# Kernel optimization log

Hardware: AMD Instinct MI355X
Metric: run time of the kernel (lower is better)

## Reference

```python
import jax, jax.numpy as jnp
import numpy as np

N = 8192
H = 512

def setup_inputs() -> dict:
    key = jax.random.key(0)
    ks = jax.random.split(key, 11)
    s = 1.0 / np.sqrt(H)
    return {
        "q": jax.random.normal(ks[0], (N, H), dtype=jnp.float32),
        "k": jax.random.normal(ks[1], (N, H), dtype=jnp.float32),
        "v": jax.random.normal(ks[2], (N, H), dtype=jnp.float32),
        "Wq": jax.random.uniform(ks[3], (H, H), jnp.float32, -s, s),
        "bq": jax.random.uniform(ks[4], (H,), jnp.float32, -s, s),
        "Wk": jax.random.uniform(ks[5], (H, H), jnp.float32, -s, s),
        "bk": jax.random.uniform(ks[6], (H,), jnp.float32, -s, s),
        "Wv": jax.random.uniform(ks[7], (H, H), jnp.float32, -s, s),
        "bv": jax.random.uniform(ks[8], (H,), jnp.float32, -s, s),
        "Wo": jax.random.uniform(ks[9], (H, H), jnp.float32, -s, s),
        "bo": jax.random.uniform(ks[10], (H,), jnp.float32, -s, s),
    }

def reference(q, k, v, Wq, bq, Wk, bk, Wv, bv, Wo, bo):
    # torch Linear: x @ W.T + b
    qp = q @ Wq.T + bq            # [N, H]
    kp = k @ Wk.T + bk            # [N, H]
    vp = v @ Wv.T + bv            # [N, H]
    weights = qp @ kp.T           # [N, N]  (no 1/sqrt(d) scaling in original)
    normalized = jax.nn.softmax(weights, axis=-1)  # [N, N]
    out = normalized @ vp         # [N, H]
    out = out @ Wo.T + bo         # [N, H]
    return (out, normalized)
```

## Files before the change

kernel.cpp:

```cpp
#include <hip/hip_runtime.h>

typedef unsigned short u16;
typedef _Float16 f16x8 __attribute__((ext_vector_type(8)));
typedef u16 u16x8 __attribute__((ext_vector_type(8)));
typedef float floatx4 __attribute__((ext_vector_type(4)));

#define DEV __device__ __forceinline__

DEV u16 f2h(float f) {
  _Float16 h = (_Float16)f;
  return __builtin_bit_cast(u16, h);
}

typedef __attribute__((address_space(3))) void lds_void_t;
typedef const __attribute__((address_space(1))) void gbl_void_t;

DEV void async16(const void* g, void* l) {
  __builtin_amdgcn_global_load_lds((gbl_void_t*)g, (lds_void_t*)l, 16, 0, 0);
}

template <int N>
DEV void wait_vm() {
  static_assert(N == 0 || N == 3 || N == 4 || N == 6 || N == 8 || N == 9 ||
                    N == 12,
                "add vmcnt literal");
  if constexpr (N == 0) asm volatile("s_waitcnt vmcnt(0)" ::: "memory");
  else if constexpr (N == 3) asm volatile("s_waitcnt vmcnt(3)" ::: "memory");
  else if constexpr (N == 4) asm volatile("s_waitcnt vmcnt(4)" ::: "memory");
  else if constexpr (N == 6) asm volatile("s_waitcnt vmcnt(6)" ::: "memory");
  else if constexpr (N == 8) asm volatile("s_waitcnt vmcnt(8)" ::: "memory");
  else if constexpr (N == 9) asm volatile("s_waitcnt vmcnt(9)" ::: "memory");
  else if constexpr (N == 12) asm volatile("s_waitcnt vmcnt(12)" ::: "memory");
}


__global__ __launch_bounds__(256) void k_cvt16(const float* __restrict__ x,
                                               u16* __restrict__ o, int n4) {
  int i = blockIdx.x * 256 + threadIdx.x;
  if (i >= n4) return;
  float4 v = ((const float4*)x)[i];
  *(ushort4*)&o[4 * (size_t)i] =
      make_ushort4(f2h(v.x), f2h(v.y), f2h(v.z), f2h(v.w));
}


__global__ __launch_bounds__(256) void k_red4(const float* __restrict__ p,
                                              size_t pstride,
                                              u16* __restrict__ o, int n4) {
  int i = blockIdx.x * 256 + threadIdx.x;
  if (i >= n4) return;
  float4 a = ((const float4*)p)[i];
  float4 b = ((const float4*)(p + pstride))[i];
  float4 c = ((const float4*)(p + 2 * pstride))[i];
  float4 d = ((const float4*)(p + 3 * pstride))[i];
  *(ushort4*)&o[4 * (size_t)i] =
      make_ushort4(f2h((a.x + b.x) + (c.x + d.x)),
                   f2h((a.y + b.y) + (c.y + d.y)),
                   f2h((a.z + b.z) + (c.z + d.z)),
                   f2h((a.w + b.w) + (c.w + d.w)));
}


__global__ __launch_bounds__(256) void k_transpose(const u16* __restrict__ in,
                                                   u16* __restrict__ out,
                                                   int R, int C) {
  __shared__ u16 T[64][72];
  int m0 = blockIdx.x * 64;
  int n0 = blockIdx.y * 64;
  int t = threadIdx.x;
#pragma unroll
  for (int i = 0; i < 2; ++i) {
    int lin = i * 2048 + t * 8;
    int r = lin >> 6, c = lin & 63;
    u16x8 d = *(const u16x8*)&in[(size_t)(m0 + r) * C + n0 + c];
#pragma unroll
    for (int j = 0; j < 8; ++j) T[r][c + j] = d[j];
  }
  __syncthreads();
#pragma unroll
  for (int i = 0; i < 2; ++i) {
    int lin = i * 2048 + t * 8;
    int r = lin >> 6, c = lin & 63;
    u16x8 d;
#pragma unroll
    for (int j = 0; j < 8; ++j) d[j] = T[c + j][r];
    *(u16x8*)&out[(size_t)(n0 + r) * R + m0 + c] = d;
  }
}


template <bool WRITEP>
__global__ __launch_bounds__(256) void k_softmax(float* __restrict__ W,
                                                 u16* __restrict__ P) {
  const size_t row = blockIdx.x;
  float4* pv = (float4*)(W + row * 8192);
  const int t = threadIdx.x;
  const int w = t >> 6, l = t & 63;
  float4 v[8];
#pragma unroll
  for (int i = 0; i < 8; ++i) v[i] = pv[i * 256 + t];
  float m = -1e30f;
#pragma unroll
  for (int i = 0; i < 8; ++i)
    m = fmaxf(m, fmaxf(fmaxf(v[i].x, v[i].y), fmaxf(v[i].z, v[i].w)));
#pragma unroll
  for (int o = 32; o >= 1; o >>= 1) m = fmaxf(m, __shfl_xor(m, o, 64));
  __shared__ float redm[4];
  __shared__ float reds[4];
  if (l == 0) redm[w] = m;
  __syncthreads();
  m = fmaxf(fmaxf(redm[0], redm[1]), fmaxf(redm[2], redm[3]));
  float s = 0.f;
#pragma unroll
  for (int i = 0; i < 8; ++i) {
    v[i].x = __expf(v[i].x - m); s += v[i].x;
    v[i].y = __expf(v[i].y - m); s += v[i].y;
    v[i].z = __expf(v[i].z - m); s += v[i].z;
    v[i].w = __expf(v[i].w - m); s += v[i].w;
  }
#pragma unroll
  for (int o = 32; o >= 1; o >>= 1) s += __shfl_xor(s, o, 64);
  if (l == 0) reds[w] = s;
  __syncthreads();
  s = (reds[0] + reds[1]) + (reds[2] + reds[3]);
  float inv = 1.0f / s;
#pragma unroll
  for (int i = 0; i < 8; ++i) {
    v[i].x *= inv; v[i].y *= inv; v[i].z *= inv; v[i].w *= inv;
    pv[i * 256 + t] = v[i];
    if constexpr (WRITEP) {
      *(ushort4*)&P[row * 8192 + (size_t)(i * 256 + t) * 4] =
          make_ushort4(f2h(v[i].x), f2h(v[i].y), f2h(v[i].z), f2h(v[i].w));
    }
  }
}


template <int BN, bool AF32, int OMODE, bool BIAS, int MINW>
__global__ __launch_bounds__(256, MINW)
void k_gemm(const void* A_, const u16* __restrict__ Bh,
            const float* __restrict__ bias, void* C_, int K, int lda, int ldb,
            int ldc, size_t zstride) {
  constexpr int NT = BN / 32;
  constexpr int BCHW = BN / 64;
  constexpr int D = 2;
  constexpr int BC = AF32 ? 1 : (D + 1);
  constexpr int LPI = 2 + BCHW;
  __shared__ alignas(16) u16 Ash[BC][128 * 32];
  __shared__ alignas(16) u16 Bsh[BC][BN * 32];

  const int m0 = blockIdx.x * 128;
  const int n0 = blockIdx.y * BN;
  const int kz = blockIdx.z * K;
  const int tid = threadIdx.x;
  const int w = tid >> 6;
  const int l = tid & 63;
  const int lr = l & 15;
  const int lq = l >> 4;
  const int wr = (w >> 1) * 64;
  const int wc = (w & 1) * (BN / 2);
  const int srow = l >> 2;
  const int scolsw = ((l & 3) ^ ((l >> 3) & 3)) * 8;
  const int sw8 = (lq ^ ((lr >> 1) & 3)) * 8;

  const u16* Ah = (const u16*)A_;
  const float* Af = (const float*)A_;

  floatx4 acc[4][NT] = {};

  if constexpr (!AF32) {
    const int nIter = K / 32;
    auto STAGE = [&](int t, int b) {
      const int k0 = kz + (t < nIter ? t : nIter - 1) * 32;
#pragma unroll
      for (int i = 0; i < 2; ++i) {
        int c = w * 2 + i;
        int row = c * 16 + srow;
        async16(Ah + (size_t)(m0 + row) * lda + k0 + scolsw, &Ash[b][c * 512]);
      }
#pragma unroll
      for (int i = 0; i < BCHW; ++i) {
        int c = w * BCHW + i;
        int row = c * 16 + srow;
        async16(Bh + (size_t)(n0 + row) * ldb + k0 + scolsw, &Bsh[b][c * 512]);
      }
    };

#pragma unroll
    for (int t = 0; t < D; ++t) STAGE(t, t);

    int bcon = 0;
    int bpro = D % BC;
    for (int t = 0; t < nIter; ++t) {
      wait_vm<LPI * (D - 1)>();
      __builtin_amdgcn_s_barrier();
      STAGE(t + D, bpro);

      f16x8 fa[4], fb[NT];
#pragma unroll
      for (int x = 0; x < 4; ++x)
        fa[x] = *(const f16x8*)&Ash[bcon][(wr + x * 16 + lr) * 32 + sw8];
#pragma unroll
      for (int x = 0; x < NT; ++x)
        fb[x] = *(const f16x8*)&Bsh[bcon][(wc + x * 16 + lr) * 32 + sw8];
#pragma unroll
      for (int mt = 0; mt < 4; ++mt)
#pragma unroll
        for (int nt = 0; nt < NT; ++nt)
          acc[mt][nt] = __builtin_amdgcn_mfma_f32_16x16x32_f16(
              fa[mt], fb[nt], acc[mt][nt], 0, 0, 0);

      if (++bcon == BC) bcon = 0;
      if (++bpro == BC) bpro = 0;
    }
  } else {
    for (int k0 = 0; k0 < K; k0 += 32) {
      __syncthreads();
#pragma unroll
      for (int i = 0; i < 2; ++i) {
        int lin = i * 2048 + tid * 8;
        int row = lin >> 5, col = lin & 31;
        const float* g = Af + (size_t)(m0 + row) * lda + k0 + col;
        float4 u0 = *(const float4*)g;
        float4 u1 = *(const float4*)(g + 4);
        u16x8 tv;
        tv[0] = f2h(u0.x); tv[1] = f2h(u0.y); tv[2] = f2h(u0.z); tv[3] = f2h(u0.w);
        tv[4] = f2h(u1.x); tv[5] = f2h(u1.y); tv[6] = f2h(u1.z); tv[7] = f2h(u1.w);
        int slot = (col >> 3) ^ ((row >> 1) & 3);
        *(u16x8*)&Ash[0][row * 32 + slot * 8] = tv;
      }
#pragma unroll
      for (int i = 0; i < BCHW; ++i) {
        int c = w * BCHW + i;
        int row = c * 16 + srow;
        async16(Bh + (size_t)(n0 + row) * ldb + k0 + scolsw, &Bsh[0][c * 512]);
      }
      __syncthreads();

      f16x8 fa[4], fb[NT];
#pragma unroll
      for (int x = 0; x < 4; ++x)
        fa[x] = *(const f16x8*)&Ash[0][(wr + x * 16 + lr) * 32 + sw8];
#pragma unroll
      for (int x = 0; x < NT; ++x)
        fb[x] = *(const f16x8*)&Bsh[0][(wc + x * 16 + lr) * 32 + sw8];
#pragma unroll
      for (int mt = 0; mt < 4; ++mt)
#pragma unroll
        for (int nt = 0; nt < NT; ++nt)
          acc[mt][nt] = __builtin_amdgcn_mfma_f32_16x16x32_f16(
              fa[mt], fb[nt], acc[mt][nt], 0, 0, 0);
    }
  }

  float bv[NT];
#pragma unroll
  for (int nt = 0; nt < NT; ++nt)
    bv[nt] = BIAS ? bias[n0 + wc + nt * 16 + lr] : 0.f;
#pragma unroll
  for (int mt = 0; mt < 4; ++mt)
#pragma unroll
    for (int nt = 0; nt < NT; ++nt)
#pragma unroll
      for (int r = 0; r < 4; ++r) {
        float x = acc[mt][nt][r] + bv[nt];
        int row = m0 + wr + mt * 16 + lq * 4 + r;
        int col = n0 + wc + nt * 16 + lr;
        size_t idx = (size_t)row * ldc + col + blockIdx.z * zstride;
        if constexpr (OMODE == 0) {
          ((float*)C_)[idx] = x;
        } else {
          ((u16*)C_)[idx] = f2h(x);
        }
      }
}


__global__ __launch_bounds__(512, 4)
void k_gemm_av(const u16* __restrict__ Ah, const u16* __restrict__ Bh,
               float* __restrict__ C_, int K, int lda, int ldb, int ldc,
               size_t zstride) {
  constexpr int D = 2;
  constexpr int BC = D + 1;
  constexpr int LPI = 3;
  __shared__ alignas(16) u16 Ash[BC][128 * 32];
  __shared__ alignas(16) u16 Bsh[BC][256 * 32];

  const int m0 = blockIdx.x * 128;
  const int n0 = blockIdx.y * 256;
  const int kz = blockIdx.z * K;
  const int tid = threadIdx.x;
  const int w = tid >> 6;
  const int l = tid & 63;
  const int lr = l & 15;
  const int lq = l >> 4;
  const int wr = (w & 1) * 64;
  const int wc = (w >> 1) * 64;
  const int srow = l >> 2;
  const int scolsw = ((l & 3) ^ ((l >> 3) & 3)) * 8;
  const int sw8 = (lq ^ ((lr >> 1) & 3)) * 8;

  floatx4 acc[4][4] = {};

  const int nIter = K / 32;
  auto STAGE = [&](int t, int b) {
    const int k0 = kz + (t < nIter ? t : nIter - 1) * 32;
    {
      int row = w * 16 + srow;
      async16(Ah + (size_t)(m0 + row) * lda + k0 + scolsw, &Ash[b][w * 512]);
    }
#pragma unroll
    for (int i = 0; i < 2; ++i) {
      int c = w * 2 + i;
      int row = c * 16 + srow;
      async16(Bh + (size_t)(n0 + row) * ldb + k0 + scolsw, &Bsh[b][c * 512]);
    }
  };

#pragma unroll
  for (int t = 0; t < D; ++t) STAGE(t, t);

  int bcon = 0;
  int bpro = D % BC;
  for (int t = 0; t < nIter; ++t) {
    wait_vm<LPI * (D - 1)>();
    __builtin_amdgcn_s_barrier();
    STAGE(t + D, bpro);

    f16x8 fa[4], fb[4];
#pragma unroll
    for (int x = 0; x < 4; ++x)
      fa[x] = *(const f16x8*)&Ash[bcon][(wr + x * 16 + lr) * 32 + sw8];
#pragma unroll
    for (int x = 0; x < 4; ++x)
      fb[x] = *(const f16x8*)&Bsh[bcon][(wc + x * 16 + lr) * 32 + sw8];
#pragma unroll
    for (int mt = 0; mt < 4; ++mt)
#pragma unroll
      for (int nt = 0; nt < 4; ++nt)
        acc[mt][nt] = __builtin_amdgcn_mfma_f32_16x16x32_f16(
            fa[mt], fb[nt], acc[mt][nt], 0, 0, 0);

    if (++bcon == BC) bcon = 0;
    if (++bpro == BC) bpro = 0;
  }

#pragma unroll
  for (int mt = 0; mt < 4; ++mt)
#pragma unroll
    for (int nt = 0; nt < 4; ++nt)
#pragma unroll
      for (int r = 0; r < 4; ++r) {
        int row = m0 + wr + mt * 16 + lq * 4 + r;
        int col = n0 + wc + nt * 16 + lr;
        C_[(size_t)row * ldc + col + blockIdx.z * zstride] = acc[mt][nt][r];
      }
}


extern "C" void kernel_launch(void* const* d_in, const int* in_sizes, int n_in,
                              void* d_out, int out_size, void* d_ws,
                              size_t ws_size, hipStream_t stream) {
  constexpr int N = 8192, H = 512;
  const float* q   = (const float*)d_in[0];
  const float* kin = (const float*)d_in[1];
  const float* v   = (const float*)d_in[2];
  const float* Wq  = (const float*)d_in[3];
  const float* bq  = (const float*)d_in[4];
  const float* Wk  = (const float*)d_in[5];
  const float* bk  = (const float*)d_in[6];
  const float* Wv  = (const float*)d_in[7];
  const float* bv  = (const float*)d_in[8];
  const float* Wo  = (const float*)d_in[9];
  const float* bo  = (const float*)d_in[10];
  float* out  = (float*)d_out;
  float* norm = out + (size_t)N * H;

  char* ws = (char*)d_ws;
  const size_t MB = 1024 * 1024;
  u16* xh   = (u16*)(ws + 0 * MB);
  u16* wb   = (u16*)(ws + 8 * MB);
  u16* qp   = (u16*)(ws + 9 * MB);
  u16* kp   = (u16*)(ws + 17 * MB);
  u16* vp   = (u16*)(ws + 25 * MB);
  u16* vpT  = (u16*)(ws + 33 * MB);
  u16* Pf   = (u16*)(ws + 41 * MB);
  float* pS = (float*)(ws + 169 * MB);
  u16* out0 = vp;

  const bool usePf    = ws_size >= 169 * MB;
  const bool useSplit = ws_size >= 233 * MB;

  dim3 blk(256);

  k_cvt16<<<4096, blk, 0, stream>>>(q, xh, (N * H) / 4);
  k_cvt16<<<256, blk, 0, stream>>>(Wq, wb, (H * H) / 4);
  k_gemm<64, false, 1, true, 2><<<dim3(64, 8), blk, 0, stream>>>(
      xh, wb, bq, qp, H, H, H, H, 0);

  k_cvt16<<<4096, blk, 0, stream>>>(kin, xh, (N * H) / 4);
  k_cvt16<<<256, blk, 0, stream>>>(Wk, wb, (H * H) / 4);
  k_gemm<64, false, 1, true, 2><<<dim3(64, 8), blk, 0, stream>>>(
      xh, wb, bk, kp, H, H, H, H, 0);

  k_cvt16<<<4096, blk, 0, stream>>>(v, xh, (N * H) / 4);
  k_cvt16<<<256, blk, 0, stream>>>(Wv, wb, (H * H) / 4);
  k_gemm<64, false, 1, true, 2><<<dim3(64, 8), blk, 0, stream>>>(
      xh, wb, bv, vp, H, H, H, H, 0);
  k_transpose<<<dim3(128, 8), blk, 0, stream>>>(vp, vpT, N, H);

  k_gemm<128, false, 0, false, 3><<<dim3(64, 64), blk, 0, stream>>>(
      qp, kp, nullptr, norm, H, H, H, N, 0);

  if (usePf)
    k_softmax<true><<<N, blk, 0, stream>>>(norm, Pf);
  else
    k_softmax<false><<<N, blk, 0, stream>>>(norm, nullptr);

  if (usePf && useSplit) {
    k_gemm_av<<<dim3(64, 2, 4), dim3(512), 0, stream>>>(
        Pf, vpT, pS, N / 4, N, N, H, (size_t)N * H);
    k_red4<<<4096, blk, 0, stream>>>(pS, (size_t)N * H, out0, (N * H) / 4);
  } else if (usePf) {
    k_gemm<64, false, 1, false, 4><<<dim3(64, 8), blk, 0, stream>>>(
        Pf, vpT, nullptr, out0, N, N, N, H, 0);
  } else {
    k_gemm<64, true, 1, false, 2><<<dim3(64, 8), blk, 0, stream>>>(
        norm, vpT, nullptr, out0, N, N, N, H, 0);
  }

  k_cvt16<<<256, blk, 0, stream>>>(Wo, wb, (H * H) / 4);
  k_gemm<64, false, 0, true, 2><<<dim3(64, 8), blk, 0, stream>>>(
      out0, wb, bo, out, H, H, H, H, 0);
}
```

Before: 682.9 us.

## Use 256x256 tile, 1024-thread GEMM for QK^T and split-K AV

Replaces the 128x256 AV GEMM kernel with a 256x256-tile, 16-wave kernel and reuses it for both the QK^T score GEMM (previously a 128-tile k_gemm) and the split-K P·V GEMM. Larger tiles raise arithmetic intensity and reduce global/L2 traffic per FLOP, and each thread now issues one A and one B async load per stage (vmcnt 2). In exchange, LDS use grows to about 96 KB per block and there are fewer blocks (1024 for QK, 256 for AV), which can lower occupancy and weaken latency hiding.

```diff
diff --git a/kernel.cpp b/kernel.cpp
--- a/kernel.cpp
+++ b/kernel.cpp
@@ -21,10 +21,11 @@
 
 template <int N>
 DEV void wait_vm() {
-  static_assert(N == 0 || N == 3 || N == 4 || N == 6 || N == 8 || N == 9 ||
-                    N == 12,
+  static_assert(N == 0 || N == 2 || N == 3 || N == 4 || N == 6 || N == 8 ||
+                    N == 9 || N == 12,
                 "add vmcnt literal");
   if constexpr (N == 0) asm volatile("s_waitcnt vmcnt(0)" ::: "memory");
+  else if constexpr (N == 2) asm volatile("s_waitcnt vmcnt(2)" ::: "memory");
   else if constexpr (N == 3) asm volatile("s_waitcnt vmcnt(3)" ::: "memory");
   else if constexpr (N == 4) asm volatile("s_waitcnt vmcnt(4)" ::: "memory");
   else if constexpr (N == 6) asm volatile("s_waitcnt vmcnt(6)" ::: "memory");
@@ -276,17 +277,17 @@
 }
 
 
-__global__ __launch_bounds__(512, 4)
-void k_gemm_av(const u16* __restrict__ Ah, const u16* __restrict__ Bh,
-               float* __restrict__ C_, int K, int lda, int ldb, int ldc,
-               size_t zstride) {
+__global__ __launch_bounds__(1024, 4)
+void k_gemm_big(const u16* __restrict__ Ah, const u16* __restrict__ Bh,
+                float* __restrict__ C_, int K, int lda, int ldb, int ldc,
+                size_t zstride) {
   constexpr int D = 2;
   constexpr int BC = D + 1;
-  constexpr int LPI = 3;
-  __shared__ alignas(16) u16 Ash[BC][128 * 32];
+  constexpr int LPI = 2;
+  __shared__ alignas(16) u16 Ash[BC][256 * 32];
   __shared__ alignas(16) u16 Bsh[BC][256 * 32];
 
-  const int m0 = blockIdx.x * 128;
+  const int m0 = blockIdx.x * 256;
   const int n0 = blockIdx.y * 256;
   const int kz = blockIdx.z * K;
   const int tid = threadIdx.x;
@@ -294,8 +295,8 @@
   const int l = tid & 63;
   const int lr = l & 15;
   const int lq = l >> 4;
-  const int wr = (w & 1) * 64;
-  const int wc = (w >> 1) * 64;
+  const int wrow = (w >> 2) * 64;
+  const int wcol = (w & 3) * 64;
   const int srow = l >> 2;
   const int scolsw = ((l & 3) ^ ((l >> 3) & 3)) * 8;
   const int sw8 = (lq ^ ((lr >> 1) & 3)) * 8;
@@ -305,16 +306,10 @@
   const int nIter = K / 32;
   auto STAGE = [&](int t, int b) {
     const int k0 = kz + (t < nIter ? t : nIter - 1) * 32;
-    {
-      int row = w * 16 + srow;
-      async16(Ah + (size_t)(m0 + row) * lda + k0 + scolsw, &Ash[b][w * 512]);
-    }
-#pragma unroll
-    for (int i = 0; i < 2; ++i) {
-      int c = w * 2 + i;
-      int row = c * 16 + srow;
-      async16(Bh + (size_t)(n0 + row) * ldb + k0 + scolsw, &Bsh[b][c * 512]);
-    }
+    async16(Ah + (size_t)(m0 + w * 16 + srow) * lda + k0 + scolsw,
+            &Ash[b][w * 512]);
+    async16(Bh + (size_t)(n0 + w * 16 + srow) * ldb + k0 + scolsw,
+            &Bsh[b][w * 512]);
   };
 
 #pragma unroll
@@ -330,10 +325,10 @@
     f16x8 fa[4], fb[4];
 #pragma unroll
     for (int x = 0; x < 4; ++x)
-      fa[x] = *(const f16x8*)&Ash[bcon][(wr + x * 16 + lr) * 32 + sw8];
+      fa[x] = *(const f16x8*)&Ash[bcon][(wrow + x * 16 + lr) * 32 + sw8];
 #pragma unroll
     for (int x = 0; x < 4; ++x)
-      fb[x] = *(const f16x8*)&Bsh[bcon][(wc + x * 16 + lr) * 32 + sw8];
+      fb[x] = *(const f16x8*)&Bsh[bcon][(wcol + x * 16 + lr) * 32 + sw8];
 #pragma unroll
     for (int mt = 0; mt < 4; ++mt)
 #pragma unroll
@@ -351,8 +346,8 @@
     for (int nt = 0; nt < 4; ++nt)
 #pragma unroll
       for (int r = 0; r < 4; ++r) {
-        int row = m0 + wr + mt * 16 + lq * 4 + r;
-        int col = n0 + wc + nt * 16 + lr;
+        int row = m0 + wrow + mt * 16 + lq * 4 + r;
+        int col = n0 + wcol + nt * 16 + lr;
         C_[(size_t)row * ldc + col + blockIdx.z * zstride] = acc[mt][nt][r];
       }
 }
@@ -409,8 +404,8 @@
       xh, wb, bv, vp, H, H, H, H, 0);
   k_transpose<<<dim3(128, 8), blk, 0, stream>>>(vp, vpT, N, H);
 
-  k_gemm<128, false, 0, false, 3><<<dim3(64, 64), blk, 0, stream>>>(
-      qp, kp, nullptr, norm, H, H, H, N, 0);
+  k_gemm_big<<<dim3(32, 32), dim3(1024), 0, stream>>>(
+      qp, kp, norm, H, H, H, N, 0);
 
   if (usePf)
     k_softmax<true><<<N, blk, 0, stream>>>(norm, Pf);
@@ -418,7 +413,7 @@
     k_softmax<false><<<N, blk, 0, stream>>>(norm, nullptr);
 
   if (usePf && useSplit) {
-    k_gemm_av<<<dim3(64, 2, 4), dim3(512), 0, stream>>>(
+    k_gemm_big<<<dim3(32, 2, 4), dim3(1024), 0, stream>>>(
         Pf, vpT, pS, N / 4, N, N, H, (size_t)N * H);
     k_red4<<<4096, blk, 0, stream>>>(pS, (size_t)N * H, out0, (N * H) / 4);
   } else if (usePf) {
```

Measured after the change: 690.6 us. No clear change (+1.1%).

## Batch QKV conversions and projections into single launches, reshuffle workspace

Applied to the files above, without the earlier changes.

The input conversions for q/k/v are merged into one three-slice kernel, and all four weight conversions into another. The three projection GEMMs become one batched launch (grid z=3) with a new dedicated 128x64-tile kernel. The workspace is repacked so the split-K attention path needs a smaller buffer, and the intermediate non-split Pf path is dropped. This cuts launch count and lets the projections fill the GPU concurrently; the cost is reusing workspace regions across stages, which depends on their lifetimes not overlapping.

```diff
diff --git a/kernel.cpp b/kernel.cpp
--- a/kernel.cpp
+++ b/kernel.cpp
@@ -21,10 +21,11 @@
 
 template <int N>
 DEV void wait_vm() {
-  static_assert(N == 0 || N == 3 || N == 4 || N == 6 || N == 8 || N == 9 ||
-                    N == 12,
+  static_assert(N == 0 || N == 2 || N == 3 || N == 4 || N == 6 || N == 8 ||
+                    N == 9 || N == 12,
                 "add vmcnt literal");
   if constexpr (N == 0) asm volatile("s_waitcnt vmcnt(0)" ::: "memory");
+  else if constexpr (N == 2) asm volatile("s_waitcnt vmcnt(2)" ::: "memory");
   else if constexpr (N == 3) asm volatile("s_waitcnt vmcnt(3)" ::: "memory");
   else if constexpr (N == 4) asm volatile("s_waitcnt vmcnt(4)" ::: "memory");
   else if constexpr (N == 6) asm volatile("s_waitcnt vmcnt(6)" ::: "memory");
@@ -34,12 +35,33 @@
 }
 
 
-__global__ __launch_bounds__(256) void k_cvt16(const float* __restrict__ x,
-                                               u16* __restrict__ o, int n4) {
+__global__ __launch_bounds__(256) void k_cvt3(const float* __restrict__ a,
+                                              const float* __restrict__ b,
+                                              const float* __restrict__ c,
+                                              u16* __restrict__ o, int n4per) {
+  int z = blockIdx.y;
+  const float* src = (z == 0) ? a : ((z == 1) ? b : c);
+  u16* dst = o + (size_t)z * n4per * 4;
   int i = blockIdx.x * 256 + threadIdx.x;
-  if (i >= n4) return;
-  float4 v = ((const float4*)x)[i];
-  *(ushort4*)&o[4 * (size_t)i] =
+  if (i >= n4per) return;
+  float4 v = ((const float4*)src)[i];
+  *(ushort4*)&dst[4 * (size_t)i] =
+      make_ushort4(f2h(v.x), f2h(v.y), f2h(v.z), f2h(v.w));
+}
+
+__global__ __launch_bounds__(256) void k_cvtw(const float* __restrict__ wq,
+                                              const float* __restrict__ wk,
+                                              const float* __restrict__ wv,
+                                              const float* __restrict__ wo_,
+                                              u16* __restrict__ w3,
+                                              u16* __restrict__ wo, int n4per) {
+  int z = blockIdx.y;
+  const float* src = (z == 0) ? wq : ((z == 1) ? wk : ((z == 2) ? wv : wo_));
+  u16* dst = (z < 3) ? (w3 + (size_t)z * n4per * 4) : wo;
+  int i = blockIdx.x * 256 + threadIdx.x;
+  if (i >= n4per) return;
+  float4 v = ((const float4*)src)[i];
+  *(ushort4*)&dst[4 * (size_t)i] =
       make_ushort4(f2h(v.x), f2h(v.y), f2h(v.z), f2h(v.w));
 }
 
@@ -272,6 +294,96 @@
         } else {
           ((u16*)C_)[idx] = f2h(x);
         }
+      }
+}
+
+
+struct Bias3 { const float* p[3]; };
+
+__global__ __launch_bounds__(256, 2)
+void k_gemm_proj(const u16* __restrict__ A3, const u16* __restrict__ W3,
+                 Bias3 b3, u16* __restrict__ C3) {
+  constexpr int H = 512;
+  constexpr int D = 2, BC = 3, LPI = 3;
+  __shared__ alignas(16) u16 Ash[BC][128 * 32];
+  __shared__ alignas(16) u16 Bsh[BC][64 * 32];
+
+  const int z = blockIdx.z;
+  const u16* Ah = A3 + (size_t)z * 8192 * H;
+  const u16* Bh = W3 + (size_t)z * H * H;
+  const float* bias = b3.p[z];
+  u16* C = C3 + (size_t)z * 8192 * H;
+
+  const int m0 = blockIdx.x * 128;
+  const int n0 = blockIdx.y * 64;
+  const int tid = threadIdx.x;
+  const int w = tid >> 6;
+  const int l = tid & 63;
+  const int lr = l & 15;
+  const int lq = l >> 4;
+  const int wr = (w >> 1) * 64;
+  const int wc = (w & 1) * 32;
+  const int srow = l >> 2;
+  const int scolsw = ((l & 3) ^ ((l >> 3) & 3)) * 8;
+  const int sw8 = (lq ^ ((lr >> 1) & 3)) * 8;
+
+  floatx4 acc[4][2] = {};
+
+  const int nIter = H / 32;
+  auto STAGE = [&](int t, int b) {
+    const int k0 = (t < nIter ? t : nIter - 1) * 32;
+#pragma unroll
+    for (int i = 0; i < 2; ++i) {
+      int c = w * 2 + i;
+      int row = c * 16 + srow;
+      async16(Ah + (size_t)(m0 + row) * H + k0 + scolsw, &Ash[b][c * 512]);
+    }
+    {
+      int row = w * 16 + srow;
+      async16(Bh + (size_t)(n0 + row) * H + k0 + scolsw, &Bsh[b][w * 512]);
+    }
+  };
+
+#pragma unroll
+  for (int t = 0; t < D; ++t) STAGE(t, t);
+
+  int bcon = 0;
+  int bpro = D % BC;
+  for (int t = 0; t < nIter; ++t) {
+    wait_vm<LPI * (D - 1)>();
+    __builtin_amdgcn_s_barrier();
+    STAGE(t + D, bpro);
+
+    f16x8 fa[4], fb[2];
+#pragma unroll
+    for (int x = 0; x < 4; ++x)
+      fa[x] = *(const f16x8*)&Ash[bcon][(wr + x * 16 + lr) * 32 + sw8];
+#pragma unroll
+    for (int x = 0; x < 2; ++x)
+      fb[x] = *(const f16x8*)&Bsh[bcon][(wc + x * 16 + lr) * 32 + sw8];
+#pragma unroll
+    for (int mt = 0; mt < 4; ++mt)
+#pragma unroll
+      for (int nt = 0; nt < 2; ++nt)
+        acc[mt][nt] = __builtin_amdgcn_mfma_f32_16x16x32_f16(
+            fa[mt], fb[nt], acc[mt][nt], 0, 0, 0);
+
+    if (++bcon == BC) bcon = 0;
+    if (++bpro == BC) bpro = 0;
+  }
+
+  float bv[2];
+#pragma unroll
+  for (int nt = 0; nt < 2; ++nt) bv[nt] = bias[n0 + wc + nt * 16 + lr];
+#pragma unroll
+  for (int mt = 0; mt < 4; ++mt)
+#pragma unroll
+    for (int nt = 0; nt < 2; ++nt)
+#pragma unroll
+      for (int r = 0; r < 4; ++r) {
+        int row = m0 + wr + mt * 16 + lq * 4 + r;
+        int col = n0 + wc + nt * 16 + lr;
+        C[(size_t)row * H + col] = f2h(acc[mt][nt][r] + bv[nt]);
       }
 }
 
@@ -378,35 +490,30 @@
 
   char* ws = (char*)d_ws;
   const size_t MB = 1024 * 1024;
-  u16* xh   = (u16*)(ws + 0 * MB);
-  u16* wb   = (u16*)(ws + 8 * MB);
-  u16* qp   = (u16*)(ws + 9 * MB);
-  u16* kp   = (u16*)(ws + 17 * MB);
-  u16* vp   = (u16*)(ws + 25 * MB);
-  u16* vpT  = (u16*)(ws + 33 * MB);
-  u16* Pf   = (u16*)(ws + 41 * MB);
-  float* pS = (float*)(ws + 169 * MB);
-  u16* out0 = vp;
-
-  const bool usePf    = ws_size >= 169 * MB;
-  const bool useSplit = ws_size >= 233 * MB;
+  u16* xh3   = (u16*)(ws + 0 * MB);
+  u16* qkv   = (u16*)(ws + 24 * MB);
+  float* pS  = (float*)(ws + 0 * MB);
+  u16* vpT   = (u16*)(ws + 64 * MB);
+  u16* wb3   = (u16*)(ws + 72 * MB);
+  u16* wbo   = (u16*)(ws + 72 * MB + 3 * (size_t)H * H * 2);
+  u16* out0  = (u16*)(ws + 74 * MB);
+  u16* Pf    = (u16*)(ws + 82 * MB);
+
+  u16* qp = qkv;
+  u16* kp = qkv + (size_t)N * H;
+  u16* vp = qkv + 2 * (size_t)N * H;
+
+  const bool usePf = ws_size >= 210 * MB;
 
   dim3 blk(256);
 
-  k_cvt16<<<4096, blk, 0, stream>>>(q, xh, (N * H) / 4);
-  k_cvt16<<<256, blk, 0, stream>>>(Wq, wb, (H * H) / 4);
-  k_gemm<64, false, 1, true, 2><<<dim3(64, 8), blk, 0, stream>>>(
-      xh, wb, bq, qp, H, H, H, H, 0);
-
-  k_cvt16<<<4096, blk, 0, stream>>>(kin, xh, (N * H) / 4);
-  k_cvt16<<<256, blk, 0, stream>>>(Wk, wb, (H * H) / 4);
-  k_gemm<64, false, 1, true, 2><<<dim3(64, 8), blk, 0, stream>>>(
-      xh, wb, bk, kp, H, H, H, H, 0);
-
-  k_cvt16<<<4096, blk, 0, stream>>>(v, xh, (N * H) / 4);
-  k_cvt16<<<256, blk, 0, stream>>>(Wv, wb, (H * H) / 4);
-  k_gemm<64, false, 1, true, 2><<<dim3(64, 8), blk, 0, stream>>>(
-      xh, wb, bv, vp, H, H, H, H, 0);
+  k_cvt3<<<dim3(4096, 3), blk, 0, stream>>>(q, kin, v, xh3, (N * H) / 4);
+  k_cvtw<<<dim3(256, 4), blk, 0, stream>>>(Wq, Wk, Wv, Wo, wb3, wbo,
+                                           (H * H) / 4);
+
+  Bias3 b3; b3.p[0] = bq; b3.p[1] = bk; b3.p[2] = bv;
+  k_gemm_proj<<<dim3(64, 8, 3), blk, 0, stream>>>(xh3, wb3, b3, qkv);
+
   k_transpose<<<dim3(128, 8), blk, 0, stream>>>(vp, vpT, N, H);
 
   k_gemm<128, false, 0, false, 3><<<dim3(64, 64), blk, 0, stream>>>(
@@ -417,19 +524,15 @@
   else
     k_softmax<false><<<N, blk, 0, stream>>>(norm, nullptr);
 
-  if (usePf && useSplit) {
+  if (usePf) {
     k_gemm_av<<<dim3(64, 2, 4), dim3(512), 0, stream>>>(
         Pf, vpT, pS, N / 4, N, N, H, (size_t)N * H);
     k_red4<<<4096, blk, 0, stream>>>(pS, (size_t)N * H, out0, (N * H) / 4);
-  } else if (usePf) {
-    k_gemm<64, false, 1, false, 4><<<dim3(64, 8), blk, 0, stream>>>(
-        Pf, vpT, nullptr, out0, N, N, N, H, 0);
   } else {
     k_gemm<64, true, 1, false, 2><<<dim3(64, 8), blk, 0, stream>>>(
         norm, vpT, nullptr, out0, N, N, N, H, 0);
   }
 
-  k_cvt16<<<256, blk, 0, stream>>>(Wo, wb, (H * H) / 4);
   k_gemm<64, false, 0, true, 2><<<dim3(64, 8), blk, 0, stream>>>(
-      out0, wb, bo, out, H, H, H, H, 0);
-}
+      out0, wbo, bo, out, H, H, H, H, 0);
+}
```

New measurement: 659.9 us. 3.4% less time.
